# Kernel optimization log

Hardware: AMD Instinct MI355X
Metric: run time of the kernel (lower is better)

The kernel has to match this reference:

```python
import jax, jax.numpy as jnp
import numpy as np

B, S, V, D, H, L = 256, 512, 32000, 100, 75, 128

def setup_inputs() -> dict:
    key = jax.random.key(0)
    ks = jax.random.split(key, 10)
    def lin(k, out_f, in_f):
        bound = 1.0 / np.sqrt(in_f)
        kw, kb = jax.random.split(k)
        W = jax.random.uniform(kw, (out_f, in_f), jnp.float32, -bound, bound)
        b = jax.random.uniform(kb, (out_f,), jnp.float32, -bound, bound)
        return W, b
    W1, b1 = lin(ks[0], H, D)   # i2h_fc1
    W2, b2 = lin(ks[1], H, H)   # i2h_fc2
    Wo, bo = lin(ks[2], H, H)   # h2o_fc
    Wfc, bfc = lin(ks[3], L, H) # fc
    emb = jax.random.normal(ks[4], (V, D), jnp.float32)
    X = jax.random.randint(ks[5], (B, S), 0, V)
    return {"X": X, "emb": emb, "W1": W1, "b1": b1, "W2": W2, "b2": b2,
            "Wo": Wo, "bo": bo, "Wfc": Wfc, "bfc": bfc}

def reference(X, emb, W1, b1, W2, b2, Wo, bo, Wfc, bfc):
    x = emb[X]                                   # [B,S,D] embedding lookup (dropout off: is_training=False)
    xp = jnp.einsum('bsd,hd->bsh', x, W1) + b1   # precompute input projection for all steps
    h0 = jnp.zeros((X.shape[0], W2.shape[0]), x.dtype)

    def step(h, xp_t):
        h = jax.nn.sigmoid(xp_t + h @ W2.T + b2)       # Elman hidden update
        o = jax.nn.sigmoid(h @ Wo.T + bo)              # per-step output
        return h, o

    _, outs = jax.lax.scan(step, h0, jnp.swapaxes(xp, 0, 1))  # [S,B,H]
    outs = jnp.swapaxes(outs, 0, 1)                            # [B,S,H] (batch_first)
    return jnp.einsum('bsh,lh->bsl', outs, Wfc) + bfc          # [B,S,L]
```

## Files before the change

kernel.cpp:

```cpp
#include <hip/hip_runtime.h>
#include <hip/hip_bf16.h>

typedef unsigned int uint;
typedef unsigned short ushort;

constexpr int Bn = 256, Sn = 512, Vn = 32000, Dn = 100, Hn = 75, Ln = 128;
constexpr int EW = 80;
constexpr int KP = 96;
constexpr int W2S = 80;

constexpr size_t OFF_EMBW = 0;
constexpr size_t OFF_HALL = OFF_EMBW + (size_t)Vn*EW;
constexpr size_t OFF_W2P  = OFF_HALL + (size_t)Bn*Sn*KP/2;
constexpr size_t OFF_WOH  = OFF_W2P + 3200;
constexpr size_t OFF_WFH  = OFF_WOH + 3840;

typedef __attribute__((ext_vector_type(2))) _Float16 half2_t;
typedef __attribute__((ext_vector_type(8))) _Float16 half8;
typedef __attribute__((ext_vector_type(4))) float floatx4;

__device__ __forceinline__ ushort f2h(float f){
    union { _Float16 h; ushort u; } v; v.h = (_Float16)f; return v.u;
}
__device__ __forceinline__ half2_t as_h2(uint u){
    union { uint u; half2_t h; } v; v.u = u; return v.h;
}
__device__ __forceinline__ float sigmoidf(float z){ return 1.f/(1.f + __expf(-z)); }

__global__ __launch_bounds__(256) void k_wprep(
    const float* __restrict__ W2, const float* __restrict__ Wo,
    const float* __restrict__ Wfc, ushort* __restrict__ w2p,
    ushort* __restrict__ woh, ushort* __restrict__ wfh, ushort* __restrict__ h_all)
{
    const int tid = blockIdx.x*256 + threadIdx.x;
    const int stride = gridDim.x*256;
    for (int i = tid; i < 80*W2S; i += stride){
        int r = i / W2S, k = i % W2S;
        w2p[i] = (r < Hn && k < Hn) ? f2h(W2[r*Hn + k]) : (ushort)0;
    }
    for (int i = tid; i < 80*KP; i += stride){
        int r = i / KP, k = i % KP;
        woh[i] = (r < Hn && k < Hn) ? f2h(Wo[r*Hn + k]) : (ushort)0;
    }
    for (int i = tid; i < Ln*KP; i += stride){
        int l = i / KP, k = i % KP;
        wfh[i] = (k < Hn) ? f2h(Wfc[l*Hn + k]) : (ushort)0;
    }
    uint* hu = (uint*)h_all;
    for (int i = tid; i < Bn*Sn*8; i += stride){
        int row = i >> 3, c = i & 7;
        hu[(size_t)row*48 + 40 + c] = 0u;
    }
}

__global__ __launch_bounds__(64) void k_embproj(
    const float* __restrict__ emb, const float* __restrict__ W1,
    const float* __restrict__ b1, const float* __restrict__ b2,
    float* __restrict__ embW)
{
    const int lane = threadIdx.x;
    const int v = blockIdx.x*64 + lane;
    const float4* ev = (const float4*)(emb + (size_t)v*Dn);
    float e[Dn];
    #pragma unroll
    for (int q = 0; q < Dn/4; ++q){
        float4 x = ev[q];
        e[4*q] = x.x; e[4*q+1] = x.y; e[4*q+2] = x.z; e[4*q+3] = x.w;
    }
    __shared__ float s_out[64*EW];
    #pragma unroll 4
    for (int j = 0; j < Hn; ++j){
        float a0 = b1[j] + b2[j], a1 = 0.f, a2 = 0.f, a3 = 0.f;
        const float* w = W1 + j*Dn;
        #pragma unroll
        for (int d = 0; d < Dn; d += 4){
            a0 += w[d]*e[d];     a1 += w[d+1]*e[d+1];
            a2 += w[d+2]*e[d+2]; a3 += w[d+3]*e[d+3];
        }
        s_out[lane*EW + j] = (a0+a1) + (a2+a3);
    }
    #pragma unroll
    for (int j = Hn; j < EW; ++j) s_out[lane*EW + j] = 0.f;
    __syncthreads();
    float* dst = embW + (size_t)blockIdx.x*64*EW;
    for (int i = lane; i < 64*EW; i += 64) dst[i] = s_out[i];
}

__global__ __launch_bounds__(64) void k_rnn(
    const int* __restrict__ X, const float* __restrict__ embW,
    const ushort* __restrict__ w2p, ushort* __restrict__ h_all)
{
    const int b = blockIdx.x;
    const int L = threadIdx.x;
    __shared__ int sX[Sn];
    __shared__ __align__(16) ushort hl[80];
    for (int i = L; i < Sn; i += 64) sX[i] = X[b*Sn + i];
    if (L < 40) ((uint*)hl)[L] = 0u;
    uint w1u[40], w2u[40];
    {
        const uint4* r1 = (const uint4*)(w2p + (size_t)L*W2S);
        int L2 = (64 + L < 80) ? (64 + L) : 79;
        const uint4* r2 = (const uint4*)(w2p + (size_t)L2*W2S);
        #pragma unroll
        for (int q = 0; q < 10; ++q){
            uint4 a = r1[q]; uint4 c = r2[q];
            w1u[4*q] = a.x; w1u[4*q+1] = a.y; w1u[4*q+2] = a.z; w1u[4*q+3] = a.w;
            w2u[4*q] = c.x; w2u[4*q+1] = c.y; w2u[4*q+2] = c.z; w2u[4*q+3] = c.w;
        }
    }
    __syncthreads();

    ushort* hout = h_all + (size_t)b*Sn*KP;
    float x1c, x2c, x1n, x2n;
    {
        int t0 = sX[0], t1 = sX[1];
        x1c = embW[(size_t)t0*EW + L];
        x2c = (L < 16) ? embW[(size_t)t0*EW + 64 + L] : 0.f;
        x1n = embW[(size_t)t1*EW + L];
        x2n = (L < 16) ? embW[(size_t)t1*EW + 64 + L] : 0.f;
    }
    for (int s = 0; s < Sn; ++s){
        uint hv[40];
        #pragma unroll
        for (int q = 0; q < 10; ++q){
            uint4 x = *(const uint4*)(hl + q*8);
            hv[4*q] = x.x; hv[4*q+1] = x.y; hv[4*q+2] = x.z; hv[4*q+3] = x.w;
        }
        int tok = sX[(s+2 < Sn) ? s+2 : Sn-1];
        float x1f = embW[(size_t)tok*EW + L];
        float x2f = (L < 16) ? embW[(size_t)tok*EW + 64 + L] : 0.f;
        float a0=0.f,a1=0.f,a2=0.f,a3=0.f, c0=0.f,c1=0.f,c2=0.f,c3=0.f;
        #pragma unroll
        for (int p = 0; p < 40; p += 4){
            a0 = __builtin_amdgcn_fdot2(as_h2(w1u[p]),   as_h2(hv[p]),   a0, false);
            a1 = __builtin_amdgcn_fdot2(as_h2(w1u[p+1]), as_h2(hv[p+1]), a1, false);
            a2 = __builtin_amdgcn_fdot2(as_h2(w1u[p+2]), as_h2(hv[p+2]), a2, false);
            a3 = __builtin_amdgcn_fdot2(as_h2(w1u[p+3]), as_h2(hv[p+3]), a3, false);
            c0 = __builtin_amdgcn_fdot2(as_h2(w2u[p]),   as_h2(hv[p]),   c0, false);
            c1 = __builtin_amdgcn_fdot2(as_h2(w2u[p+1]), as_h2(hv[p+1]), c1, false);
            c2 = __builtin_amdgcn_fdot2(as_h2(w2u[p+2]), as_h2(hv[p+2]), c2, false);
            c3 = __builtin_amdgcn_fdot2(as_h2(w2u[p+3]), as_h2(hv[p+3]), c3, false);
        }
        float h1 = sigmoidf(((a0+a1)+(a2+a3)) + x1c);
        float h2 = sigmoidf(((c0+c1)+(c2+c3)) + x2c);
        if (L >= 11) h2 = 0.f;
        ushort u1 = f2h(h1);
        hl[L] = u1;
        hout[(size_t)s*KP + L] = u1;
        if (L < 16){
            ushort u2 = f2h(h2);
            hl[64 + L] = u2;
            hout[(size_t)s*KP + 64 + L] = u2;
        }
        x1c = x1n; x2c = x2n; x1n = x1f; x2n = x2f;
    }
}

__global__ __launch_bounds__(256) void k_out(
    const ushort* __restrict__ h_all, const ushort* __restrict__ woh,
    const ushort* __restrict__ wfh, const float* __restrict__ bo,
    const float* __restrict__ bfc, float* __restrict__ out)
{
    const int lane = threadIdx.x & 63;
    const int w    = threadIdx.x >> 6;
    const size_t r0 = (size_t)blockIdx.x*64 + w*16;
    const int m = lane & 15;
    const int g = lane >> 4;
    __shared__ __align__(16) ushort o_lds[4][16*104];
    ushort* ot = o_lds[w];
    for (int i = lane; i < 128; i += 64){
        int row = i >> 3, cw = i & 7;
        *(uint*)&ot[row*104 + 80 + cw*2] = 0u;
    }
    floatx4 acc1[5] = {};
    const ushort* hbase = h_all + r0*KP;
    #pragma unroll
    for (int ks = 0; ks < 3; ++ks){
        half8 a = *(const half8*)(hbase + (size_t)m*KP + ks*32 + g*8);
        #pragma unroll
        for (int t = 0; t < 5; ++t){
            half8 bt = *(const half8*)(woh + (16*t + m)*KP + ks*32 + g*8);
            acc1[t] = __builtin_amdgcn_mfma_f32_16x16x32_f16(a, bt, acc1[t], 0, 0, 0);
        }
    }
    #pragma unroll
    for (int t = 0; t < 5; ++t){
        int n = 16*t + m;
        float bias = (n < Hn) ? bo[n] : 0.f;
        #pragma unroll
        for (int r = 0; r < 4; ++r){
            int row = g*4 + r;
            float o = sigmoidf(acc1[t][r] + bias);
            if (n >= Hn) o = 0.f;
            ot[row*104 + n] = f2h(o);
        }
    }
    floatx4 acc2[8] = {};
    #pragma unroll
    for (int ks = 0; ks < 3; ++ks){
        half8 a = *(const half8*)(ot + m*104 + ks*32 + g*8);
        #pragma unroll
        for (int t = 0; t < 8; ++t){
            half8 bt = *(const half8*)(wfh + (16*t + m)*KP + ks*32 + g*8);
            acc2[t] = __builtin_amdgcn_mfma_f32_16x16x32_f16(a, bt, acc2[t], 0, 0, 0);
        }
    }
    float* orow = out + r0*Ln;
    #pragma unroll
    for (int t = 0; t < 8; ++t){
        float bias = bfc[16*t + m];
        #pragma unroll
        for (int r = 0; r < 4; ++r){
            int row = g*4 + r;
            orow[(size_t)row*Ln + 16*t + m] = acc2[t][r] + bias;
        }
    }
}

extern "C" void kernel_launch(void* const* d_in, const int* in_sizes, int n_in,
                              void* d_out, int out_size, void* d_ws, size_t ws_size,
                              hipStream_t stream)
{
    const int*   X   = (const int*)d_in[0];
    const float* emb = (const float*)d_in[1];
    const float* W1  = (const float*)d_in[2];
    const float* b1  = (const float*)d_in[3];
    const float* W2  = (const float*)d_in[4];
    const float* b2  = (const float*)d_in[5];
    const float* Wo  = (const float*)d_in[6];
    const float* bo  = (const float*)d_in[7];
    const float* Wfc = (const float*)d_in[8];
    const float* bfc = (const float*)d_in[9];
    float* out = (float*)d_out;
    float* ws  = (float*)d_ws;

    float*  embW = ws + OFF_EMBW;
    ushort* hall = (ushort*)(ws + OFF_HALL);
    ushort* w2p  = (ushort*)(ws + OFF_W2P);
    ushort* woh  = (ushort*)(ws + OFF_WOH);
    ushort* wfh  = (ushort*)(ws + OFF_WFH);

    k_wprep<<<dim3(512), dim3(256), 0, stream>>>(W2, Wo, Wfc, w2p, woh, wfh, hall);
    k_embproj<<<dim3(Vn/64), dim3(64), 0, stream>>>(emb, W1, b1, b2, embW);
    k_rnn<<<dim3(Bn), dim3(64), 0, stream>>>(X, embW, w2p, hall);
    k_out<<<dim3((Bn*Sn)/64), dim3(256), 0, stream>>>(hall, woh, wfh, bo, bfc, out);
}
```

Before: 392.8 us.

## Broadcast RNN hidden state via DPP and readlane instead of LDS

```diff
diff --git a/kernel.cpp b/kernel.cpp
--- a/kernel.cpp
+++ b/kernel.cpp
@@ -86,16 +86,14 @@
     for (int i = lane; i < 64*EW; i += 64) dst[i] = s_out[i];
 }
 
-__global__ __launch_bounds__(64) void k_rnn(
+__global__ __launch_bounds__(64, 1) void k_rnn(
     const int* __restrict__ X, const float* __restrict__ embW,
     const ushort* __restrict__ w2p, ushort* __restrict__ h_all)
 {
     const int b = blockIdx.x;
     const int L = threadIdx.x;
     __shared__ int sX[Sn];
-    __shared__ __align__(16) ushort hl[80];
     for (int i = L; i < Sn; i += 64) sX[i] = X[b*Sn + i];
-    if (L < 40) ((uint*)hl)[L] = 0u;
     uint w1u[40], w2u[40];
     {
         const uint4* r1 = (const uint4*)(w2p + (size_t)L*W2S);
@@ -119,39 +117,43 @@
         x1n = embW[(size_t)t1*EW + L];
         x2n = (L < 16) ? embW[(size_t)t1*EW + 64 + L] : 0.f;
     }
+    uint hp[40];
+    #pragma unroll
+    for (int q = 0; q < 40; ++q) hp[q] = 0u;
+
+    #pragma unroll 2
     for (int s = 0; s < Sn; ++s){
-        uint hv[40];
-        #pragma unroll
-        for (int q = 0; q < 10; ++q){
-            uint4 x = *(const uint4*)(hl + q*8);
-            hv[4*q] = x.x; hv[4*q+1] = x.y; hv[4*q+2] = x.z; hv[4*q+3] = x.w;
-        }
         int tok = sX[(s+2 < Sn) ? s+2 : Sn-1];
         float x1f = embW[(size_t)tok*EW + L];
         float x2f = (L < 16) ? embW[(size_t)tok*EW + 64 + L] : 0.f;
-        float a0=0.f,a1=0.f,a2=0.f,a3=0.f, c0=0.f,c1=0.f,c2=0.f,c3=0.f;
+        float a0=x1c,a1=0.f,a2=0.f,a3=0.f, c0=x2c,c1=0.f,c2=0.f,c3=0.f;
         #pragma unroll
         for (int p = 0; p < 40; p += 4){
-            a0 = __builtin_amdgcn_fdot2(as_h2(w1u[p]),   as_h2(hv[p]),   a0, false);
-            a1 = __builtin_amdgcn_fdot2(as_h2(w1u[p+1]), as_h2(hv[p+1]), a1, false);
-            a2 = __builtin_amdgcn_fdot2(as_h2(w1u[p+2]), as_h2(hv[p+2]), a2, false);
-            a3 = __builtin_amdgcn_fdot2(as_h2(w1u[p+3]), as_h2(hv[p+3]), a3, false);
-            c0 = __builtin_amdgcn_fdot2(as_h2(w2u[p]),   as_h2(hv[p]),   c0, false);
-            c1 = __builtin_amdgcn_fdot2(as_h2(w2u[p+1]), as_h2(hv[p+1]), c1, false);
-            c2 = __builtin_amdgcn_fdot2(as_h2(w2u[p+2]), as_h2(hv[p+2]), c2, false);
-            c3 = __builtin_amdgcn_fdot2(as_h2(w2u[p+3]), as_h2(hv[p+3]), c3, false);
-        }
-        float h1 = sigmoidf(((a0+a1)+(a2+a3)) + x1c);
-        float h2 = sigmoidf(((c0+c1)+(c2+c3)) + x2c);
+            a0 = __builtin_amdgcn_fdot2(as_h2(w1u[p]),   as_h2(hp[p]),   a0, false);
+            a1 = __builtin_amdgcn_fdot2(as_h2(w1u[p+1]), as_h2(hp[p+1]), a1, false);
+            a2 = __builtin_amdgcn_fdot2(as_h2(w1u[p+2]), as_h2(hp[p+2]), a2, false);
+            a3 = __builtin_amdgcn_fdot2(as_h2(w1u[p+3]), as_h2(hp[p+3]), a3, false);
+            c0 = __builtin_amdgcn_fdot2(as_h2(w2u[p]),   as_h2(hp[p]),   c0, false);
+            c1 = __builtin_amdgcn_fdot2(as_h2(w2u[p+1]), as_h2(hp[p+1]), c1, false);
+            c2 = __builtin_amdgcn_fdot2(as_h2(w2u[p+2]), as_h2(hp[p+2]), c2, false);
+            c3 = __builtin_amdgcn_fdot2(as_h2(w2u[p+3]), as_h2(hp[p+3]), c3, false);
+        }
+        float h1 = sigmoidf((a0+a1)+(a2+a3));
+        float h2 = sigmoidf((c0+c1)+(c2+c3));
         if (L >= 11) h2 = 0.f;
         ushort u1 = f2h(h1);
-        hl[L] = u1;
+        ushort u2 = f2h(h2);
         hout[(size_t)s*KP + L] = u1;
-        if (L < 16){
-            ushort u2 = f2h(h2);
-            hl[64 + L] = u2;
-            hout[(size_t)s*KP + 64 + L] = u2;
-        }
+        if (L < 16) hout[(size_t)s*KP + 64 + L] = u2;
+        uint v1 = u1, v2 = u2;
+        uint pr1 = (uint)__builtin_amdgcn_update_dpp(0, (int)v1, 0xB1, 0xF, 0xF, true);
+        uint pr2 = (uint)__builtin_amdgcn_update_dpp(0, (int)v2, 0xB1, 0xF, 0xF, true);
+        uint q1 = v1 | (pr1 << 16);
+        uint q2 = v2 | (pr2 << 16);
+        #pragma unroll
+        for (int q = 0; q < 32; ++q) hp[q] = (uint)__builtin_amdgcn_readlane((int)q1, 2*q);
+        #pragma unroll
+        for (int q = 0; q < 8; ++q)  hp[32+q] = (uint)__builtin_amdgcn_readlane((int)q2, 2*q);
         x1c = x1n; x2c = x2n; x1n = x1f; x2n = x2f;
     }
 }
```

Result: slower. 402.0 us (+2.4%).
